# Performance work log

Hardware: AMD Instinct MI355X
Metric: run time of the kernel (lower is better)

The kernel has to match this reference:

```python
import jax, jax.numpy as jnp
import numpy as np

N = 1048576
D = 128
C = 1000
MOMENTUM = 0.95


def setup_inputs() -> dict:
    key = jax.random.key(0)
    k1, k2, k3, k4 = jax.random.split(key, 4)
    feats = jax.random.normal(k1, (N, D), dtype=jnp.float32)
    labels = jax.random.randint(k2, (N,), 0, C, dtype=jnp.int64)
    weights = jax.random.uniform(k3, (N,), dtype=jnp.float32)
    proto = jax.random.normal(k4, (C, D), dtype=jnp.float32)  # buffer [C, d]
    return {"feats": feats, "labels": labels, "weights": weights, "proto": proto}


def reference(feats, labels, weights, proto):
    # Per-class weighted mean via a single segment reduction (replaces the
    # per-class masked loop in the torch module), then fused EMA update.
    labels = labels.astype(jnp.int32)
    # [C, d] sum of w_i * f_i per class
    wsum_feats = jax.ops.segment_sum(weights[:, None] * feats, labels, num_segments=C)
    # [C] sum of weights per class
    wsum = jax.ops.segment_sum(weights, labels, num_segments=C)
    vec = wsum_feats / jnp.maximum(wsum, 1e-8)[:, None]  # [C, d]
    present = (wsum > 0.0)[:, None]  # classes seen in this batch
    new_proto = jnp.where(present, MOMENTUM * proto + (1.0 - MOMENTUM) * vec, proto)
    return new_proto
```

## Files before the change

### kernel.cpp

```cpp
#include <hip/hip_runtime.h>

#define NROWS 1048576
#define DIM   128
#define NCLS  1000
#define NBLK  256
#define RPB   4096
#define RPT   16
#define MOM   0.95f


__global__ __launch_bounds__(256) void k_hist(const int* __restrict__ labels,
                                              unsigned* __restrict__ total,
                                              unsigned* __restrict__ blockCnt)
{
    __shared__ unsigned h[1024];
    const int tid = threadIdx.x;
    const int b   = blockIdx.x;
    for (int c = tid; c < 1024; c += 256) h[c] = 0u;
    __syncthreads();
    const int base = b * RPB;
#pragma unroll
    for (int k = 0; k < RPT; ++k)
        atomicAdd(&h[labels[base + k * 256 + tid]], 1u);
    __syncthreads();
    for (int c = tid; c < 1024; c += 256) {
        const unsigned cnt = h[c];
        blockCnt[b * 1024 + c] = cnt;
        if (cnt) atomicAdd(&total[c], cnt);
    }
}

__global__ __launch_bounds__(1024) void k_scan(const unsigned* __restrict__ total,
                                               unsigned* __restrict__ classBase)
{
    __shared__ unsigned s[1024];
    const int tid = threadIdx.x;
    unsigned v = (tid < NCLS) ? total[tid] : 0u;
    s[tid] = v;
    __syncthreads();
    for (int off = 1; off < 1024; off <<= 1) {
        unsigned u = (tid >= off) ? s[tid - off] : 0u;
        __syncthreads();
        s[tid] += u;
        __syncthreads();
    }
    if (tid < NCLS) classBase[tid] = s[tid] - v;
}

__global__ __launch_bounds__(256) void k_scanB(const unsigned* __restrict__ blockCnt,
                                               const unsigned* __restrict__ classBase,
                                               unsigned* __restrict__ blockBase)
{
    __shared__ unsigned s[256];
    const int c = blockIdx.x;
    const int t = threadIdx.x;
    unsigned v = blockCnt[t * 1024 + c];
    s[t] = v;
    __syncthreads();
    for (int off = 1; off < 256; off <<= 1) {
        unsigned u = (t >= off) ? s[t - off] : 0u;
        __syncthreads();
        s[t] += u;
        __syncthreads();
    }
    blockBase[t * 1024 + c] = classBase[c] + (s[t] - v);
}

__global__ __launch_bounds__(256) void k_scatter(const int* __restrict__ labels,
                                                 const unsigned* __restrict__ blockBase,
                                                 unsigned* __restrict__ perm)
{
    __shared__ unsigned h[1024];
    __shared__ unsigned localBase[1024];
    __shared__ unsigned basec[1024];
    __shared__ unsigned tsum[256];
    __shared__ unsigned s_perm[RPB];
    __shared__ unsigned short s_cls[RPB];

    const int tid = threadIdx.x;
    const int b   = blockIdx.x;

    for (int c = tid; c < 1024; c += 256) {
        h[c]     = 0u;
        basec[c] = blockBase[b * 1024 + c];
    }
    __syncthreads();

    const int base = b * RPB;
    int lab[RPT];
#pragma unroll
    for (int k = 0; k < RPT; ++k) {
        lab[k] = labels[base + k * 256 + tid];
        atomicAdd(&h[lab[k]], 1u);
    }
    __syncthreads();

    const unsigned a0 = h[4*tid], a1 = h[4*tid+1], a2 = h[4*tid+2], a3 = h[4*tid+3];
    const unsigned ts = a0 + a1 + a2 + a3;
    tsum[tid] = ts;
    __syncthreads();
    for (int off = 1; off < 256; off <<= 1) {
        unsigned u = (tid >= off) ? tsum[tid - off] : 0u;
        __syncthreads();
        tsum[tid] += u;
        __syncthreads();
    }
    const unsigned eb = tsum[tid] - ts;
    localBase[4*tid]   = eb;
    localBase[4*tid+1] = eb + a0;
    localBase[4*tid+2] = eb + a0 + a1;
    localBase[4*tid+3] = eb + a0 + a1 + a2;
    h[4*tid] = 0u; h[4*tid+1] = 0u; h[4*tid+2] = 0u; h[4*tid+3] = 0u;
    __syncthreads();

#pragma unroll
    for (int k = 0; k < RPT; ++k) {
        const int c = lab[k];
        const unsigned pos = localBase[c] + atomicAdd(&h[c], 1u);
        s_perm[pos] = (unsigned)(base + k * 256 + tid);
        s_cls[pos]  = (unsigned short)c;
    }
    __syncthreads();

    for (int pos = tid; pos < RPB; pos += 256) {
        const int c = s_cls[pos];
        perm[basec[c] + (pos - localBase[c])] = s_perm[pos];
    }
}

__global__ __launch_bounds__(256) void k_reduce(
        const float*    __restrict__ feats,
        const float*    __restrict__ weights,
        const float*    __restrict__ proto,
        const unsigned* __restrict__ perm,
        const unsigned* __restrict__ total,
        const unsigned* __restrict__ classBase,
        float* __restrict__ out)
{
    const int c      = blockIdx.x;
    const int tid    = threadIdx.x;
    const int lane32 = tid & 31;
    const int grp    = tid >> 5;
    const int n      = (int)total[c];
    const unsigned base = classBase[c];
    const float4* __restrict__ f4 = (const float4*)feats;

    float4 acc = make_float4(0.f, 0.f, 0.f, 0.f);
    float  wacc = 0.f;

    int i = grp;
    for (; i + 24 < n; i += 32) {
        unsigned r0 = perm[base + i];
        unsigned r1 = perm[base + i + 8];
        unsigned r2 = perm[base + i + 16];
        unsigned r3 = perm[base + i + 24];
        float w0 = weights[r0], w1 = weights[r1];
        float w2 = weights[r2], w3 = weights[r3];
        float4 f0 = f4[(long)r0 * 32 + lane32];
        float4 f1 = f4[(long)r1 * 32 + lane32];
        float4 f2 = f4[(long)r2 * 32 + lane32];
        float4 f3 = f4[(long)r3 * 32 + lane32];
        acc.x += w0 * f0.x; acc.y += w0 * f0.y; acc.z += w0 * f0.z; acc.w += w0 * f0.w;
        acc.x += w1 * f1.x; acc.y += w1 * f1.y; acc.z += w1 * f1.z; acc.w += w1 * f1.w;
        acc.x += w2 * f2.x; acc.y += w2 * f2.y; acc.z += w2 * f2.z; acc.w += w2 * f2.w;
        acc.x += w3 * f3.x; acc.y += w3 * f3.y; acc.z += w3 * f3.z; acc.w += w3 * f3.w;
        wacc += w0 + w1 + w2 + w3;
    }
    for (; i < n; i += 8) {
        unsigned r = perm[base + i];
        float w = weights[r];
        float4 f = f4[(long)r * 32 + lane32];
        acc.x += w * f.x; acc.y += w * f.y; acc.z += w * f.z; acc.w += w * f.w;
        wacc += w;
    }

    __shared__ float4 sAcc[8][32];
    __shared__ float  sW[8];
    sAcc[grp][lane32] = acc;
    if (lane32 == 0) sW[grp] = wacc;
    __syncthreads();

    if (grp == 0) {
        float4 t = sAcc[0][lane32];
#pragma unroll
        for (int g = 1; g < 8; ++g) {
            float4 a = sAcc[g][lane32];
            t.x += a.x; t.y += a.y; t.z += a.z; t.w += a.w;
        }
        float ws = 0.f;
#pragma unroll
        for (int g = 0; g < 8; ++g) ws += sW[g];

        const float4 p = ((const float4*)proto)[c * 32 + lane32];
        float4 o;
        if (ws > 0.f) {
            const float den = fmaxf(ws, 1e-8f);
            o.x = MOM * p.x + 0.05f * (t.x / den);
            o.y = MOM * p.y + 0.05f * (t.y / den);
            o.z = MOM * p.z + 0.05f * (t.z / den);
            o.w = MOM * p.w + 0.05f * (t.w / den);
        } else {
            o = p;
        }
        ((float4*)out)[c * 32 + lane32] = o;
    }
}

extern "C" void kernel_launch(void* const* d_in, const int* in_sizes, int n_in,
                              void* d_out, int out_size, void* d_ws, size_t ws_size,
                              hipStream_t stream)
{
    const float* feats   = (const float*)d_in[0];
    const int*   labels  = (const int*)  d_in[1];
    const float* weights = (const float*)d_in[2];
    const float* proto   = (const float*)d_in[3];
    float* out = (float*)d_out;

    unsigned* total     = (unsigned*)d_ws;
    unsigned* classBase = total + 1024;
    unsigned* blockCnt  = classBase + 1024;
    unsigned* blockBase = blockCnt + NBLK * 1024;
    unsigned* perm      = blockBase + NBLK * 1024;

    hipMemsetAsync(total, 0, 1024 * sizeof(unsigned), stream);
    k_hist   <<<NBLK, 256, 0, stream>>>(labels, total, blockCnt);
    k_scan   <<<1, 1024, 0, stream>>>(total, classBase);
    k_scanB  <<<NCLS, 256, 0, stream>>>(blockCnt, classBase, blockBase);
    k_scatter<<<NBLK, 256, 0, stream>>>(labels, blockBase, perm);
    k_reduce <<<NCLS, 256, 0, stream>>>(feats, weights, proto, perm,
                                        total, classBase, out);
}
```

Before: 717.6 us.

## Merge class and block scans into one kernel, transpose block counts, vectorize label loads

```diff
diff --git a/kernel.cpp b/kernel.cpp
--- a/kernel.cpp
+++ b/kernel.cpp
@@ -11,63 +11,68 @@
 
 __global__ __launch_bounds__(256) void k_hist(const int* __restrict__ labels,
                                               unsigned* __restrict__ total,
-                                              unsigned* __restrict__ blockCnt)
+                                              unsigned* __restrict__ blockCntT)
 {
     __shared__ unsigned h[1024];
     const int tid = threadIdx.x;
     const int b   = blockIdx.x;
     for (int c = tid; c < 1024; c += 256) h[c] = 0u;
     __syncthreads();
-    const int base = b * RPB;
-#pragma unroll
-    for (int k = 0; k < RPT; ++k)
-        atomicAdd(&h[labels[base + k * 256 + tid]], 1u);
+    const int rbase = b * RPB + tid * RPT;
+    const int4* __restrict__ l4 = (const int4*)(labels + rbase);
+#pragma unroll
+    for (int k = 0; k < 4; ++k) {
+        const int4 v = l4[k];
+        atomicAdd(&h[v.x], 1u); atomicAdd(&h[v.y], 1u);
+        atomicAdd(&h[v.z], 1u); atomicAdd(&h[v.w], 1u);
+    }
     __syncthreads();
     for (int c = tid; c < 1024; c += 256) {
         const unsigned cnt = h[c];
-        blockCnt[b * 1024 + c] = cnt;
+        blockCntT[c * NBLK + b] = cnt;
         if (cnt) atomicAdd(&total[c], cnt);
     }
 }
 
-__global__ __launch_bounds__(1024) void k_scan(const unsigned* __restrict__ total,
-                                               unsigned* __restrict__ classBase)
-{
-    __shared__ unsigned s[1024];
-    const int tid = threadIdx.x;
-    unsigned v = (tid < NCLS) ? total[tid] : 0u;
-    s[tid] = v;
-    __syncthreads();
-    for (int off = 1; off < 1024; off <<= 1) {
-        unsigned u = (tid >= off) ? s[tid - off] : 0u;
-        __syncthreads();
-        s[tid] += u;
-        __syncthreads();
-    }
-    if (tid < NCLS) classBase[tid] = s[tid] - v;
-}
-
-__global__ __launch_bounds__(256) void k_scanB(const unsigned* __restrict__ blockCnt,
-                                               const unsigned* __restrict__ classBase,
-                                               unsigned* __restrict__ blockBase)
-{
-    __shared__ unsigned s[256];
+__global__ __launch_bounds__(256) void k_bases(const unsigned* __restrict__ total,
+                                               const unsigned* __restrict__ blockCntT,
+                                               unsigned* __restrict__ classBase,
+                                               unsigned* __restrict__ blockBaseT)
+{
     const int c = blockIdx.x;
     const int t = threadIdx.x;
-    unsigned v = blockCnt[t * 1024 + c];
-    s[t] = v;
+    __shared__ unsigned sred[8];
+    __shared__ unsigned sscan[256];
+
+    unsigned partial = 0;
+#pragma unroll
+    for (int k = 0; k < 4; ++k) {
+        const int j = t * 4 + k;
+        if (j < c) partial += total[j];
+    }
+#pragma unroll
+    for (int off = 32; off; off >>= 1) partial += __shfl_down(partial, off);
+    if ((t & 63) == 0) sred[t >> 6] = partial;
+    __syncthreads();
+    if (t == 0) sred[4] = sred[0] + sred[1] + sred[2] + sred[3];
+    __syncthreads();
+    const unsigned cb = sred[4];
+
+    const unsigned v = blockCntT[c * NBLK + t];
+    sscan[t] = v;
     __syncthreads();
     for (int off = 1; off < 256; off <<= 1) {
-        unsigned u = (t >= off) ? s[t - off] : 0u;
-        __syncthreads();
-        s[t] += u;
-        __syncthreads();
-    }
-    blockBase[t * 1024 + c] = classBase[c] + (s[t] - v);
+        unsigned u = (t >= off) ? sscan[t - off] : 0u;
+        __syncthreads();
+        sscan[t] += u;
+        __syncthreads();
+    }
+    blockBaseT[c * NBLK + t] = cb + (sscan[t] - v);
+    if (t == 0) classBase[c] = cb;
 }
 
 __global__ __launch_bounds__(256) void k_scatter(const int* __restrict__ labels,
-                                                 const unsigned* __restrict__ blockBase,
+                                                 const unsigned* __restrict__ blockBaseT,
                                                  unsigned* __restrict__ perm)
 {
     __shared__ unsigned h[1024];
@@ -82,17 +87,20 @@
 
     for (int c = tid; c < 1024; c += 256) {
         h[c]     = 0u;
-        basec[c] = blockBase[b * 1024 + c];
-    }
-    __syncthreads();
-
-    const int base = b * RPB;
+        basec[c] = blockBaseT[c * NBLK + b];
+    }
+    __syncthreads();
+
+    const int rbase = b * RPB + tid * RPT;
+    const int4* __restrict__ l4 = (const int4*)(labels + rbase);
     int lab[RPT];
 #pragma unroll
-    for (int k = 0; k < RPT; ++k) {
-        lab[k] = labels[base + k * 256 + tid];
-        atomicAdd(&h[lab[k]], 1u);
-    }
+    for (int k = 0; k < 4; ++k) {
+        const int4 v = l4[k];
+        lab[4*k] = v.x; lab[4*k+1] = v.y; lab[4*k+2] = v.z; lab[4*k+3] = v.w;
+    }
+#pragma unroll
+    for (int k = 0; k < RPT; ++k) atomicAdd(&h[lab[k]], 1u);
     __syncthreads();
 
     const unsigned a0 = h[4*tid], a1 = h[4*tid+1], a2 = h[4*tid+2], a3 = h[4*tid+3];
@@ -117,7 +125,7 @@
     for (int k = 0; k < RPT; ++k) {
         const int c = lab[k];
         const unsigned pos = localBase[c] + atomicAdd(&h[c], 1u);
-        s_perm[pos] = (unsigned)(base + k * 256 + tid);
+        s_perm[pos] = (unsigned)(rbase + k);
         s_cls[pos]  = (unsigned short)c;
     }
     __syncthreads();
@@ -216,17 +224,16 @@
     const float* proto   = (const float*)d_in[3];
     float* out = (float*)d_out;
 
-    unsigned* total     = (unsigned*)d_ws;
-    unsigned* classBase = total + 1024;
-    unsigned* blockCnt  = classBase + 1024;
-    unsigned* blockBase = blockCnt + NBLK * 1024;
-    unsigned* perm      = blockBase + NBLK * 1024;
+    unsigned* total      = (unsigned*)d_ws;
+    unsigned* classBase  = total + 1024;
+    unsigned* blockCntT  = classBase + 1024;
+    unsigned* blockBaseT = blockCntT + 1024 * NBLK;
+    unsigned* perm       = blockBaseT + 1024 * NBLK;
 
     hipMemsetAsync(total, 0, 1024 * sizeof(unsigned), stream);
-    k_hist   <<<NBLK, 256, 0, stream>>>(labels, total, blockCnt);
-    k_scan   <<<1, 1024, 0, stream>>>(total, classBase);
-    k_scanB  <<<NCLS, 256, 0, stream>>>(blockCnt, classBase, blockBase);
-    k_scatter<<<NBLK, 256, 0, stream>>>(labels, blockBase, perm);
+    k_hist   <<<NBLK, 256, 0, stream>>>(labels, total, blockCntT);
+    k_bases  <<<NCLS, 256, 0, stream>>>(total, blockCntT, classBase, blockBaseT);
+    k_scatter<<<NBLK, 256, 0, stream>>>(labels, blockBaseT, perm);
     k_reduce <<<NCLS, 256, 0, stream>>>(feats, weights, proto, perm,
                                         total, classBase, out);
 }
```

Result: no change. 710.3 us (-1.0%).
